# Optimization experiments

Measured on AMD Instinct MI355X. Metric: run time of the kernel, lower is better.

Reference implementation:

```python
import math
import jax, jax.numpy as jnp
import numpy as np

D, DK, DV = 256, 256, 256

def setup_inputs() -> dict:
    key = jax.random.key(0)
    ks = jax.random.split(key, 7)
    s = 1.0 / math.sqrt(D)
    return {
        "x": jax.random.normal(ks[0], (4, 4096, D), dtype=jnp.float32),
        "Wq": jax.random.uniform(ks[1], (D, DK), jnp.float32, -s, s),
        "bq": jax.random.uniform(ks[2], (DK,), jnp.float32, -s, s),
        "Wk": jax.random.uniform(ks[3], (D, DK), jnp.float32, -s, s),
        "bk": jax.random.uniform(ks[4], (DK,), jnp.float32, -s, s),
        "Wv": jax.random.uniform(ks[5], (D, DV), jnp.float32, -s, s),
        "bv": jax.random.uniform(ks[6], (DV,), jnp.float32, -s, s),
    }

def reference(x, Wq, bq, Wk, bk, Wv, bv):
    # x: [B, S, D]
    q = x @ Wq + bq            # [B, S, DK]
    k = x @ Wk + bk            # [B, S, DK]
    v = x @ Wv + bv            # [B, S, DV]
    scores = jnp.einsum('bqd,bkd->bqk', q, k) / math.sqrt(DK)  # [B, S, S]
    S = x.shape[1]
    causal = jnp.tril(jnp.ones((S, S), dtype=bool))  # True = keep
    scores = jnp.where(causal, scores, -jnp.inf)
    attn = jax.nn.softmax(scores, axis=-1)
    return jnp.einsum('bqk,bkd->bqd', attn, v)  # [B, S, DV]
```

## Files before the change

### kernel.cpp

```cpp
#include <hip/hip_runtime.h>
#include <cmath>

#define LOG2E 1.4426950408889634f

typedef __attribute__((ext_vector_type(8))) __bf16 bf16x8;
typedef __attribute__((ext_vector_type(4))) float f32x4;
typedef __attribute__((ext_vector_type(16))) float f32x16;
typedef __attribute__((ext_vector_type(4))) float float4v;
typedef __attribute__((ext_vector_type(8))) unsigned short ushort8;
typedef __attribute__((ext_vector_type(4))) unsigned int uint4v;
typedef __attribute__((ext_vector_type(2))) int int2v;

__device__ __forceinline__ unsigned short f2bf(float f) {
  unsigned int u = __builtin_bit_cast(unsigned int, f);
  u += 0x7fffu + ((u >> 16) & 1u);
  return (unsigned short)(u >> 16);
}

__device__ __forceinline__ unsigned int cvtpk(float lo, float hi) {
  unsigned int r;
  asm volatile("v_cvt_pk_bf16_f32 %0, %1, %2" : "=v"(r) : "v"(lo), "v"(hi));
  return r;
}

__device__ __forceinline__ void gload_lds16(const unsigned short* g, unsigned short* l) {
  __builtin_amdgcn_global_load_lds(
      (const __attribute__((address_space(1))) unsigned int*)(const void*)g,
      (__attribute__((address_space(3))) unsigned int*)(void*)l, 16, 0, 0);
}

__global__ __launch_bounds__(256) void prep_w_kernel(
    const float* __restrict__ Wq, const float* __restrict__ Wk,
    const float* __restrict__ Wv, unsigned short* __restrict__ Wt) {
  const int w = blockIdx.y, n = blockIdx.x, k = threadIdx.x;
  const float* W = (w == 0) ? Wq : ((w == 1) ? Wk : Wv);
  const float s = (w == 0) ? (LOG2E / 16.0f) : 1.0f;
  Wt[w * 65536 + n * 256 + k] = f2bf(W[k * 256 + n] * s);
}

__global__ __launch_bounds__(256) void proj_kernel(
    const float* __restrict__ x, const unsigned short* __restrict__ Wt,
    const float* __restrict__ bq, const float* __restrict__ bk,
    const float* __restrict__ bv,
    unsigned short* __restrict__ q_o, unsigned short* __restrict__ k_o,
    unsigned short* __restrict__ vt_o) {
  const int mt = blockIdx.x;
  const int tid = threadIdx.x;
  const int wid = tid >> 6, lane = tid & 63, g = (lane >> 4) & 3, c = lane & 15;
  const int row_base = mt * 64 + wid * 16;

  bf16x8 a[8];
  const float* xr = x + (size_t)(row_base + c) * 256;
#pragma unroll
  for (int s = 0; s < 8; ++s) {
    const float4v v0 = *(const float4v*)(xr + s * 32 + g * 8);
    const float4v v1 = *(const float4v*)(xr + s * 32 + g * 8 + 4);
    union { bf16x8 v; unsigned short u[8]; } t;
#pragma unroll
    for (int j = 0; j < 4; ++j) { t.u[j] = f2bf(v0[j]); t.u[4 + j] = f2bf(v1[j]); }
    a[s] = t.v;
  }

  const unsigned short* w0 = Wt;
  const unsigned short* w1 = Wt + 65536;
  const unsigned short* w2 = Wt + 131072;

#pragma unroll
  for (int nf = 0; nf < 16; ++nf) {
    f32x4 aq = (f32x4){0.f, 0.f, 0.f, 0.f};
    f32x4 ak = (f32x4){0.f, 0.f, 0.f, 0.f};
    f32x4 av = (f32x4){0.f, 0.f, 0.f, 0.f};
    const unsigned short* r0 = w0 + (size_t)(nf * 16 + c) * 256;
    const unsigned short* r1 = w1 + (size_t)(nf * 16 + c) * 256;
    const unsigned short* r2 = w2 + (size_t)(nf * 16 + c) * 256;
#pragma unroll
    for (int s = 0; s < 8; ++s) {
      bf16x8 b0 = *(const bf16x8*)(r0 + s * 32 + g * 8);
      bf16x8 b1 = *(const bf16x8*)(r1 + s * 32 + g * 8);
      bf16x8 b2 = *(const bf16x8*)(r2 + s * 32 + g * 8);
      aq = __builtin_amdgcn_mfma_f32_16x16x32_bf16(a[s], b0, aq, 0, 0, 0);
      ak = __builtin_amdgcn_mfma_f32_16x16x32_bf16(a[s], b1, ak, 0, 0, 0);
      av = __builtin_amdgcn_mfma_f32_16x16x32_bf16(a[s], b2, av, 0, 0, 0);
    }
    const float bql = bq[nf * 16 + c] * (LOG2E / 16.0f);
    const float bkl = bk[nf * 16 + c];
    const float bvl = bv[nf * 16 + c];
#pragma unroll
    for (int r = 0; r < 4; ++r) {
      const int row = row_base + g * 4 + r;
      q_o[(size_t)row * 256 + nf * 16 + c] = f2bf(aq[r] + bql);
      k_o[(size_t)row * 256 + nf * 16 + c] = f2bf(ak[r] + bkl);
      const int b_ = row >> 12, s_ = row & 4095;
      vt_o[((size_t)b_ * 256 + nf * 16 + c) * 4096 + s_] = f2bf(av[r] + bvl);
    }
  }
}

__global__ __launch_bounds__(256, 2) void attn_kernel(
    const unsigned short* __restrict__ qg, const unsigned short* __restrict__ kg,
    const unsigned short* __restrict__ vtg, float* __restrict__ out) {
  __shared__ unsigned short Klds[64 * 256];
  __shared__ unsigned short Vlds[256 * 64];
  __shared__ float llds[2][32];

  const int tid = threadIdx.x;
  const int wid = tid >> 6, lane = tid & 63;
  const int hi = lane >> 5, q5 = lane & 31;
  const int wk = wid & 1, dh = wid >> 1;
  const int bid = blockIdx.x;
  const int half = bid >> 8, k6 = (bid >> 2) & 63, b = bid & 3;
  const int qt = half ? k6 : 127 - k6;
  const int T = (qt >> 1) + 1;

  const unsigned short* qb = qg + (size_t)b * 4096 * 256;
  const unsigned short* kb = kg + (size_t)b * 4096 * 256;
  const unsigned short* vb = vtg + (size_t)b * 256 * 4096;
  float* outb = out + (size_t)b * 4096 * 256;

  const int q0 = qt * 32;
  const int qrow = q0 + q5;

  int koff[8], voff[8];
#pragma unroll
  for (int i = 0; i < 8; ++i) {
    const int kr = wid * 16 + i * 2 + (lane >> 5);
    const int c8 = (lane & 31) ^ (kr & 7);
    koff[i] = kr * 256 + c8 * 8;
    const int d = wid * 64 + i * 8 + (lane >> 3);
    const int c8v = (lane & 7) ^ (d & 7);
    voff[i] = d * 4096 + c8v * 8;
  }

  auto stage = [&](int t) {
    const unsigned short* kp = kb + t * (64 * 256);
    const unsigned short* vp = vb + t * 64;
#pragma unroll
    for (int i = 0; i < 8; ++i)
      gload_lds16(kp + koff[i], &Klds[(wid * 8 + i) * 512]);
#pragma unroll
    for (int i = 0; i < 8; ++i)
      gload_lds16(vp + voff[i], &Vlds[(wid * 8 + i) * 512]);
  };

  bf16x8 bqf[16];
  {
    const unsigned short* qr = qb + (size_t)qrow * 256;
#pragma unroll
    for (int s = 0; s < 16; ++s) bqf[s] = *(const bf16x8*)(qr + s * 16 + hi * 8);
  }

  float l = 0.f;
  f32x16 o[4];
#pragma unroll
  for (int d = 0; d < 4; ++d)
#pragma unroll
    for (int r = 0; r < 16; ++r) o[d][r] = 0.f;

  const int krow = wk * 32 + q5;
  const int ksw = (krow & 7) << 3;
  const int kbase = krow * 256;

  int kcolr[16];
#pragma unroll
  for (int r = 0; r < 16; ++r) kcolr[r] = wk * 32 + (r & 3) + 8 * (r >> 2) + 4 * hi;

  stage(0);
  for (int t = 0; t < T; ++t) {
    __syncthreads();

    f32x16 sa, sb;
#pragma unroll
    for (int r = 0; r < 16; ++r) { sa[r] = 0.f; sb[r] = 0.f; }
#pragma unroll
    for (int s = 0; s < 8; ++s) {
      bf16x8 ka0 = *(const bf16x8*)(&Klds[(kbase + s * 16 + hi * 8) ^ ksw]);
      bf16x8 ka1 = *(const bf16x8*)(&Klds[(kbase + (s + 8) * 16 + hi * 8) ^ ksw]);
      sa = __builtin_amdgcn_mfma_f32_32x32x16_bf16(ka0, bqf[s], sa, 0, 0, 0);
      sb = __builtin_amdgcn_mfma_f32_32x32x16_bf16(ka1, bqf[s + 8], sb, 0, 0, 0);
    }
    f32x16 sc = sa + sb;

    if (t == T - 1) {
#pragma unroll
      for (int r = 0; r < 16; ++r)
        if (t * 64 + kcolr[r] > qrow) sc[r] = -1e30f;
    }

    float p[16];
#pragma unroll
    for (int r = 0; r < 16; ++r) p[r] = __builtin_amdgcn_exp2f(sc[r]);
    {
      float s0 = (p[0] + p[1]) + (p[2] + p[3]);
      float s1 = (p[4] + p[5]) + (p[6] + p[7]);
      float s2 = (p[8] + p[9]) + (p[10] + p[11]);
      float s3 = (p[12] + p[13]) + (p[14] + p[15]);
      l += (s0 + s1) + (s2 + s3);
    }

    bf16x8 pfrag[2];
#pragma unroll
    for (int s2 = 0; s2 < 2; ++s2) {
      const int base = s2 * 8;
      unsigned int X = cvtpk(p[base + 0], p[base + 1]);
      unsigned int Y = cvtpk(p[base + 2], p[base + 3]);
      unsigned int Z = cvtpk(p[base + 4], p[base + 5]);
      unsigned int W = cvtpk(p[base + 6], p[base + 7]);
#if __has_builtin(__builtin_amdgcn_permlane32_swap)
      int2v rx = __builtin_amdgcn_permlane32_swap((int)X, (int)Z, false, false);
      int2v ry = __builtin_amdgcn_permlane32_swap((int)Y, (int)W, false, false);
      uint4v u = (uint4v){(unsigned)rx[0], (unsigned)ry[0], (unsigned)rx[1], (unsigned)ry[1]};
#else
      const unsigned int Xp = __shfl_xor((int)X, 32);
      const unsigned int Yp = __shfl_xor((int)Y, 32);
      const unsigned int Zp = __shfl_xor((int)Z, 32);
      const unsigned int Wp = __shfl_xor((int)W, 32);
      uint4v u = (uint4v){hi ? Zp : X, hi ? Wp : Y, hi ? Z : Xp, hi ? W : Yp};
#endif
      pfrag[s2] = __builtin_bit_cast(bf16x8, u);
    }

#pragma unroll
    for (int dblk = 0; dblk < 4; ++dblk) {
      const int drow = (dh * 4 + dblk) * 32 + q5;
      const int vsw = (drow & 7) << 3;
      const int vbase = drow * 64 + wk * 32;
#pragma unroll
      for (int s2 = 0; s2 < 2; ++s2) {
        bf16x8 va = *(const bf16x8*)(&Vlds[(vbase + s2 * 16 + hi * 8) ^ vsw]);
        o[dblk] = __builtin_amdgcn_mfma_f32_32x32x16_bf16(va, pfrag[s2], o[dblk], 0, 0, 0);
      }
    }

    if (t + 1 < T) {
      __syncthreads();
      stage(t + 1);
    }
  }

  l += __shfl_xor(l, 32);
  if (dh == 0 && hi == 0) llds[wk][q5] = l;
  __syncthreads();
  const float L = llds[0][q5] + llds[1][q5];
  const float scale = 1.0f / L;

  float* oz = (float*)Klds;
  if (wk == 1) {
#pragma unroll
    for (int dblk = 0; dblk < 4; ++dblk)
#pragma unroll
      for (int r = 0; r < 16; ++r) {
        const int dg = (dh * 4 + dblk) * 32 + (r & 3) + 8 * (r >> 2) + 4 * hi;
        oz[dg * 32 + q5] = o[dblk][r];
      }
  }
  __syncthreads();
  if (wk == 0) {
#pragma unroll
    for (int dblk = 0; dblk < 4; ++dblk) {
#pragma unroll
      for (int q2 = 0; q2 < 4; ++q2) {
        float4v val;
#pragma unroll
        for (int e = 0; e < 4; ++e) {
          const int r = q2 * 4 + e;
          const int dg = (dh * 4 + dblk) * 32 + e + 8 * q2 + 4 * hi;
          val[e] = (o[dblk][r] + oz[dg * 32 + q5]) * scale;
        }
        *(float4v*)(outb + (size_t)qrow * 256 + (dh * 4 + dblk) * 32 + 8 * q2 + 4 * hi) = val;
      }
    }
  }
}

extern "C" void kernel_launch(void* const* d_in, const int* in_sizes, int n_in,
                              void* d_out, int out_size, void* d_ws, size_t ws_size,
                              hipStream_t stream) {
  (void)in_sizes; (void)n_in; (void)out_size; (void)ws_size;
  const float* x  = (const float*)d_in[0];
  const float* Wq = (const float*)d_in[1];
  const float* bq = (const float*)d_in[2];
  const float* Wk = (const float*)d_in[3];
  const float* bk = (const float*)d_in[4];
  const float* Wv = (const float*)d_in[5];
  const float* bv = (const float*)d_in[6];
  float* out = (float*)d_out;

  unsigned short* qs  = (unsigned short*)d_ws;
  unsigned short* ks  = qs  + (size_t)16384 * 256;
  unsigned short* vts = ks  + (size_t)16384 * 256;
  unsigned short* Wt  = vts + (size_t)16384 * 256;

  prep_w_kernel<<<dim3(256, 3), 256, 0, stream>>>(Wq, Wk, Wv, Wt);
  proj_kernel<<<256, 256, 0, stream>>>(x, Wt, bq, bk, bv, qs, ks, vts);
  attn_kernel<<<512, 256, 0, stream>>>(qs, ks, vts, out);
}
```

Baseline: 173.1 us.

## Split projection over column halves and stage V transpose through LDS

The projection kernel now runs on a 2D grid, with each block computing half of the output columns, so twice as many blocks are available to fill the GPU. The transposed V output is first written into a padded shared-memory tile and then stored with 16-byte vectorized writes along the sequence dimension. This replaces the previous scattered 2-byte strided stores. The cost is that each block reloads and converts its rows of x, which doubles x reads, and it adds an LDS tile plus a barrier.

```diff
diff --git a/kernel.cpp b/kernel.cpp
--- a/kernel.cpp
+++ b/kernel.cpp
@@ -7,8 +7,8 @@
 typedef __attribute__((ext_vector_type(4))) float f32x4;
 typedef __attribute__((ext_vector_type(16))) float f32x16;
 typedef __attribute__((ext_vector_type(4))) float float4v;
-typedef __attribute__((ext_vector_type(8))) unsigned short ushort8;
 typedef __attribute__((ext_vector_type(4))) unsigned int uint4v;
+typedef __attribute__((ext_vector_type(8))) unsigned short ushort8v;
 typedef __attribute__((ext_vector_type(2))) int int2v;
 
 __device__ __forceinline__ unsigned short f2bf(float f) {
@@ -44,7 +44,10 @@
     const float* __restrict__ bv,
     unsigned short* __restrict__ q_o, unsigned short* __restrict__ k_o,
     unsigned short* __restrict__ vt_o) {
+  __shared__ unsigned short vlds[128 * 72];
+
   const int mt = blockIdx.x;
+  const int nfh = blockIdx.y;
   const int tid = threadIdx.x;
   const int wid = tid >> 6, lane = tid & 63, g = (lane >> 4) & 3, c = lane & 15;
   const int row_base = mt * 64 + wid * 16;
@@ -66,7 +69,8 @@
   const unsigned short* w2 = Wt + 131072;
 
 #pragma unroll
-  for (int nf = 0; nf < 16; ++nf) {
+  for (int nfi = 0; nfi < 8; ++nfi) {
+    const int nf = nfh * 8 + nfi;
     f32x4 aq = (f32x4){0.f, 0.f, 0.f, 0.f};
     f32x4 ak = (f32x4){0.f, 0.f, 0.f, 0.f};
     f32x4 av = (f32x4){0.f, 0.f, 0.f, 0.f};
@@ -90,9 +94,21 @@
       const int row = row_base + g * 4 + r;
       q_o[(size_t)row * 256 + nf * 16 + c] = f2bf(aq[r] + bql);
       k_o[(size_t)row * 256 + nf * 16 + c] = f2bf(ak[r] + bkl);
-      const int b_ = row >> 12, s_ = row & 4095;
-      vt_o[((size_t)b_ * 256 + nf * 16 + c) * 4096 + s_] = f2bf(av[r] + bvl);
-    }
+      vlds[(nfi * 16 + c) * 72 + (wid * 16 + g * 4 + r)] = f2bf(av[r] + bvl);
+    }
+  }
+
+  __syncthreads();
+
+  const int bb = mt >> 6;
+  const int s0 = (mt & 63) * 64;
+  unsigned short* vout = vt_o + ((size_t)bb * 256 + nfh * 128) * 4096 + s0;
+#pragma unroll
+  for (int it = 0; it < 4; ++it) {
+    const int idx = it * 256 + tid;
+    const int dl = idx >> 3, s8 = idx & 7;
+    ushort8v val = *(const ushort8v*)(vlds + dl * 72 + s8 * 8);
+    *(ushort8v*)(vout + (size_t)dl * 4096 + s8 * 8) = val;
   }
 }
 
@@ -108,8 +124,8 @@
   const int hi = lane >> 5, q5 = lane & 31;
   const int wk = wid & 1, dh = wid >> 1;
   const int bid = blockIdx.x;
-  const int half = bid >> 8, k6 = (bid >> 2) & 63, b = bid & 3;
-  const int qt = half ? k6 : 127 - k6;
+  const int half = bid >> 8, c = bid & 255, b = c & 3;
+  const int qt = half ? (c >> 2) : (127 - (c >> 2));
   const int T = (qt >> 1) + 1;
 
   const unsigned short* qb = qg + (size_t)b * 4096 * 256;
@@ -117,8 +133,7 @@
   const unsigned short* vb = vtg + (size_t)b * 256 * 4096;
   float* outb = out + (size_t)b * 4096 * 256;
 
-  const int q0 = qt * 32;
-  const int qrow = q0 + q5;
+  const int qrow = qt * 32 + q5;
 
   int koff[8], voff[8];
 #pragma unroll
@@ -132,7 +147,7 @@
   }
 
   auto stage = [&](int t) {
-    const unsigned short* kp = kb + t * (64 * 256);
+    const unsigned short* kp = kb + (size_t)t * 16384;
     const unsigned short* vp = vb + t * 64;
 #pragma unroll
     for (int i = 0; i < 8; ++i)
@@ -291,6 +306,6 @@
   unsigned short* Wt  = vts + (size_t)16384 * 256;
 
   prep_w_kernel<<<dim3(256, 3), 256, 0, stream>>>(Wq, Wk, Wv, Wt);
-  proj_kernel<<<256, 256, 0, stream>>>(x, Wt, bq, bk, bv, qs, ks, vts);
+  proj_kernel<<<dim3(256, 2), 256, 0, stream>>>(x, Wt, bq, bk, bv, qs, ks, vts);
   attn_kernel<<<512, 256, 0, stream>>>(qs, ks, vts, out);
 }
```

Result: faster. 166.9 us (-3.6%).
